# Performance work log

Hardware: AMD Instinct MI355X
Metric: run time of the kernel (lower is better)

The kernel has to match this reference:

```python
import jax, jax.numpy as jnp
import numpy as np

B, H, N, D = 16, 8, 256, 32


def setup_inputs() -> dict:
    key = jax.random.key(0)
    k1, k2, k3 = jax.random.split(key, 3)
    q = jax.random.normal(k1, (B, H, N, D), dtype=jnp.float32)
    k = jax.random.normal(k2, (B, H, N, D), dtype=jnp.float32)
    scale = jnp.ones((1,), dtype=jnp.float32)  # unused by the module
    mask = jnp.zeros((B, 1, N, N), dtype=bool)  # True == masked out
    # learned attention vector, xavier_uniform over (1, H, 1, 1, D)
    fan = 1 * H * 1 * 1 * D
    bound = float(np.sqrt(6.0 / (1 + D)))  # xavier for (..., D) param
    attention = jax.random.uniform(k3, (1, H, 1, 1, D), dtype=jnp.float32,
                                   minval=-bound, maxval=bound)
    return {"q": q, "k": k, "scale": scale, "mask": mask, "attention": attention}


def reference(q, k, scale, mask, attention):
    # summed: [B, H, Nq, Nk, D] via broadcast of q.unsqueeze(-2)+k.unsqueeze(-3)
    summed = q[:, :, :, None, :] + k[:, :, None, :, :]
    # GATv2 score: a^T * silu(q_i + k_j), reduced over head_dim
    scores = jnp.sum(jax.nn.silu(summed) * attention, axis=-1)  # [B, H, Nq, Nk]
    neg = jnp.finfo(scores.dtype).min
    scores_masked = jnp.where(mask, neg, scores)
    attn = jax.nn.softmax(scores_masked, axis=-1)
    return attn
```

## Files before the change

### kernel.cpp

```cpp
#include <hip/hip_runtime.h>
#include <stdint.h>
#include <stddef.h>

constexpr int Bc = 16, Hc = 8, Nc = 256, Dc = 32;
constexpr float LOG2E = 1.44269504088896340736f;

constexpr int    MF    = 10;
constexpr double PHALF = 9.7;
constexpr double LFIT  = 9.0;

constexpr double PI_ = 3.14159265358979323846;

constexpr double cexp_(double x) {
    int n = (int)(x >= 0 ? x + 0.5 : x - 0.5);
    double f = x - n, t = 1.0, s = 1.0;
    for (int i = 1; i <= 26; ++i) { t *= f / i; s += t; }
    const double E = 2.71828182845904523536;
    double en = 1.0, bb = n >= 0 ? E : 1.0 / E;
    int an = n < 0 ? -n : n;
    for (int i = 0; i < an; ++i) en *= bb;
    return s * en;
}
constexpr double creduce_(double x) {
    while (x >  PI_) x -= 2.0 * PI_;
    while (x < -PI_) x += 2.0 * PI_;
    return x;
}
constexpr double ccos_(double x0) {
    double x = creduce_(x0), x2 = x * x, t = 1.0, s = 1.0;
    for (int i = 1; i <= 16; ++i) { t *= -x2 / ((2.0*i - 1.0) * (2.0*i)); s += t; }
    return s;
}
constexpr double csin_(double x0) {
    double x = creduce_(x0), x2 = x * x, t = x, s = x;
    for (int i = 1; i <= 16; ++i) { t *= -x2 / ((2.0*i) * (2.0*i + 1.0)); s += t; }
    return s;
}
constexpr double Gfun_(double x) {
    double z = x < 0 ? -x : x;
    double e = cexp_(z);
    return 0.5 * z * ((e - 1.0) / (e + 1.0));
}
constexpr double csqrt_(double x) {
    if (x <= 0) return 0;
    double r = x > 1 ? x : 1;
    for (int i = 0; i < 40; ++i) r = 0.5 * (r + x / r);
    return r;
}

struct FitT { float tk[MF + 1]; float tq[MF + 1]; };

constexpr FitT lsFit_() {
    constexpr int NB = MF + 1;
    double A[NB][NB] = {}, bv[NB] = {};
    for (int p = 0; p < NB; ++p)
        for (int qq = 0; qq < NB; ++qq) {
            double wm = (p - qq) * PI_ / PHALF, wp = (p + qq) * PI_ / PHALF;
            double Sm = (p == qq)     ? LFIT : csin_(wm * LFIT) / wm;
            double Sp = (p + qq == 0) ? LFIT : csin_(wp * LFIT) / wp;
            A[p][qq] = 0.5 * (Sm + Sp);
        }
    constexpr int NS = 128;
    double hh = LFIT / NS, gx[NS + 1] = {};
    for (int i = 0; i <= NS; ++i) gx[i] = Gfun_(i * hh);
    for (int p = 0; p < NB; ++p) {
        double s = 0;
        for (int i = 0; i <= NS; ++i) {
            double wgt = (i == 0 || i == NS) ? 1.0 : ((i & 1) ? 4.0 : 2.0);
            s += wgt * gx[i] * ccos_(p * PI_ / PHALF * (i * hh));
        }
        bv[p] = s * hh / 3.0;
    }
    for (int p = 0; p < NB; ++p) A[p][p] += 1e-8 * LFIT;
    for (int col = 0; col < NB; ++col) {
        int piv = col; double best = A[col][col] < 0 ? -A[col][col] : A[col][col];
        for (int r = col + 1; r < NB; ++r) {
            double v = A[r][col] < 0 ? -A[r][col] : A[r][col];
            if (v > best) { best = v; piv = r; }
        }
        if (piv != col) {
            for (int cc = 0; cc < NB; ++cc) { double t = A[col][cc]; A[col][cc] = A[piv][cc]; A[piv][cc] = t; }
            double t = bv[col]; bv[col] = bv[piv]; bv[piv] = t;
        }
        for (int r = col + 1; r < NB; ++r) {
            double f = A[r][col] / A[col][col];
            for (int cc = col; cc < NB; ++cc) A[r][cc] -= f * A[col][cc];
            bv[r] -= f * bv[col];
        }
    }
    double c[NB] = {};
    for (int r = NB - 1; r >= 0; --r) {
        double s = bv[r];
        for (int cc = r + 1; cc < NB; ++cc) s -= A[r][cc] * c[cc];
        c[r] = s / A[r][r];
    }
    FitT f{};
    for (int m = 0; m <= MF; ++m) {
        double rt = csqrt_(c[m] < 0 ? -c[m] : c[m]);
        f.tk[m] = (float)rt;
        f.tq[m] = (float)(c[m] < 0 ? -rt : rt);
    }
    return f;
}
constexpr FitT CF = lsFit_();

typedef _Float16 half8  __attribute__((ext_vector_type(8)));
typedef float    f32x16 __attribute__((ext_vector_type(16)));

__device__ __forceinline__ uint32_t pkh_(float a, float b) {
    auto v = __builtin_amdgcn_cvt_pkrtz(a, b);
    uint32_t u; __builtin_memcpy(&u, &v, 4); return u;
}

__device__ __forceinline__ void dma16(const char* g, char* l) {
    __builtin_amdgcn_global_load_lds(
        (const __attribute__((address_space(1))) unsigned int*)(g),
        (__attribute__((address_space(3))) unsigned int*)(l),
        16, 0, 0);
}

constexpr int    KCH      = Nc * 128;
constexpr size_t KF_BYTES = (size_t)Bc * Hc * MF * KCH;
constexpr size_t AK_OFF   = KF_BYTES;

__global__ __launch_bounds__(256) void feat_kernel(
    const float* __restrict__ k, const float* __restrict__ att,
    char* __restrict__ kf, float* __restrict__ akg)
{
    const int gid = blockIdx.x * 256 + threadIdx.x;
    const int u  = gid & 7;
    const int j  = (gid >> 3) & (Nc - 1);
    const int bh = gid >> 11;
    const int h  = bh & (Hc - 1);
    const float4 kv = *(const float4*)(k + ((size_t)bh * Nc + j) * Dc + 4 * u);
    const float4 a4 = *(const float4*)(att + h * Dc + 4 * u);
    float part = a4.x * kv.x + a4.y * kv.y + a4.z * kv.z + a4.w * kv.w;
    part += __shfl_xor(part, 1, 64);
    part += __shfl_xor(part, 2, 64);
    part += __shfl_xor(part, 4, 64);
    if (u == 0) akg[bh * Nc + j] = part;

    const float invTwoP = (float)(1.0 / (2.0 * PHALF));
    float c1[4], s1[4], cm[4], sm[4];
    const float rv[4] = { kv.x, kv.y, kv.z, kv.w };
#pragma unroll
    for (int c = 0; c < 4; ++c) {
        float r = __builtin_amdgcn_fractf(rv[c] * invTwoP);
        c1[c] = __builtin_amdgcn_cosf(r);
        s1[c] = __builtin_amdgcn_sinf(r);
        cm[c] = c1[c]; sm[c] = s1[c];
    }
    char* base = kf + (size_t)bh * (MF * KCH) + j * 128 + ((u ^ (j & 7)) << 4);
#pragma unroll
    for (int m = 1; m <= MF; ++m) {
        const float tk = CF.tk[m];
        uint4 wv;
        wv.x = pkh_(tk * cm[0], tk * sm[0]);
        wv.y = pkh_(tk * cm[1], tk * sm[1]);
        wv.z = pkh_(tk * cm[2], tk * sm[2]);
        wv.w = pkh_(tk * cm[3], tk * sm[3]);
        *(uint4*)(base + (size_t)(m - 1) * KCH) = wv;
        if (m < MF) {
#pragma unroll
            for (int e = 0; e < 4; ++e) {
                float cn = fmaf(c1[e], cm[e], -(s1[e] * sm[e]));
                float sn = fmaf(s1[e], cm[e],   c1[e] * sm[e]);
                cm[e] = cn; sm[e] = sn;
            }
        }
    }
}

constexpr int QCH   = 128 * 128;
constexpr int QBASE = 2 * KCH;
constexpr int SRED  = QBASE + 2 * QCH;
constexpr int SMEM2 = SRED + 2048;

__global__ __launch_bounds__(512, 2) void gatv2_gemm_kernel(
    const float* __restrict__ q, const uint8_t* __restrict__ mask,
    const float* __restrict__ att, const char* __restrict__ kf,
    const float* __restrict__ akg, float* __restrict__ out)
{
    extern __shared__ char smem[];
    float* sred = (float*)(smem + SRED);
    const int tid = threadIdx.x, lane = tid & 63, w = tid >> 6;
    const int bh = blockIdx.y, h = bh & 7, b = bh >> 3;
    const int iBlk = blockIdx.x * 128;
    const float invTwoP = (float)(1.0 / (2.0 * PHALF));

    const int dq = tid & 7, rw = tid >> 3;
    const float4 a4 = *(const float4*)(att + h * Dc + 4 * dq);
    float qc1[8], qs1[8], qcm[8], qsm[8];
    int offQ[2];
#pragma unroll
    for (int it = 0; it < 2; ++it) {
        const int i = rw + it * 64;
        const float4 qv = *(const float4*)(q + ((size_t)bh * Nc + iBlk + i) * Dc + 4 * dq);
        const float rv[4] = { qv.x, qv.y, qv.z, qv.w };
#pragma unroll
        for (int c = 0; c < 4; ++c) {
            float r = __builtin_amdgcn_fractf(rv[c] * invTwoP);
            qc1[4*it+c] = __builtin_amdgcn_cosf(r);
            qs1[4*it+c] = __builtin_amdgcn_sinf(r);
            qcm[4*it+c] = qc1[4*it+c];
            qsm[4*it+c] = qs1[4*it+c];
        }
        offQ[it] = QBASE + i * 128 + ((dq ^ (i & 7)) << 4);
    }

    const char* kg = kf + (size_t)bh * (MF * KCH) + w * 4096 + lane * 16;

    auto dmaK = [&](int mIdx, int buf) {
        const char* g = kg + (size_t)mIdx * KCH;
        char* l = smem + buf * KCH + w * 4096;
#pragma unroll
        for (int t = 0; t < 4; ++t)
            dma16(g + t * 1024, l + t * 1024);
    };

    auto buildQ = [&](int m, int buf) {
        const float g0 = CF.tq[m]*a4.x, g1 = CF.tq[m]*a4.y;
        const float g2 = CF.tq[m]*a4.z, g3 = CF.tq[m]*a4.w;
#pragma unroll
        for (int it = 0; it < 2; ++it) {
            uint4 wv;
            wv.x = pkh_(g0*qcm[4*it+0], -(g0*qsm[4*it+0]));
            wv.y = pkh_(g1*qcm[4*it+1], -(g1*qsm[4*it+1]));
            wv.z = pkh_(g2*qcm[4*it+2], -(g2*qsm[4*it+2]));
            wv.w = pkh_(g3*qcm[4*it+3], -(g3*qsm[4*it+3]));
            *(uint4*)(smem + buf * QCH + offQ[it]) = wv;
        }
        if (m < MF) {
#pragma unroll
            for (int e = 0; e < 8; ++e) {
                float cn = fmaf(qc1[e], qcm[e], -(qs1[e] * qsm[e]));
                float sn = fmaf(qs1[e], qcm[e],   qc1[e] * qsm[e]);
                qcm[e] = cn; qsm[e] = sn;
            }
        }
    };

    const int hi5 = lane >> 5, col = lane & 31;
    const int wi = w & 1, wj = w >> 1;
    const int baseA0 = QBASE + (wi*64 + col) * 128, baseA1 = baseA0 + 32*128;
    const int baseB0 = (wj*64 + col) * 128,         baseB1 = baseB0 + 32*128;
    const int sA = col & 7;

    f32x16 acc[2][2];
#pragma unroll
    for (int a2 = 0; a2 < 2; ++a2)
#pragma unroll
        for (int b2 = 0; b2 < 2; ++b2)
#pragma unroll
            for (int e = 0; e < 16; ++e) acc[a2][b2][e] = 0.0f;

    auto mfmaC = [&](int buf) {
        const int qb = buf * QCH, kb = buf * KCH;
#pragma unroll
        for (int s = 0; s < 4; ++s) {
            const int du = ((2*s + hi5) ^ sA) << 4;
            half8 A0 = *(const half8*)(smem + qb + baseA0 + du);
            half8 A1 = *(const half8*)(smem + qb + baseA1 + du);
            half8 B0 = *(const half8*)(smem + kb + baseB0 + du);
            half8 B1 = *(const half8*)(smem + kb + baseB1 + du);
            acc[0][0] = __builtin_amdgcn_mfma_f32_32x32x16_f16(A0, B0, acc[0][0], 0, 0, 0);
            acc[0][1] = __builtin_amdgcn_mfma_f32_32x32x16_f16(A0, B1, acc[0][1], 0, 0, 0);
            acc[1][0] = __builtin_amdgcn_mfma_f32_32x32x16_f16(A1, B0, acc[1][0], 0, 0, 0);
            acc[1][1] = __builtin_amdgcn_mfma_f32_32x32x16_f16(A1, B1, acc[1][1], 0, 0, 0);
        }
    };

    buildQ(1, 0);
    dmaK(0, 0);
    __syncthreads();
#pragma unroll
    for (int m = 1; m <= MF; ++m) {
        const int cur = (m - 1) & 1;
        if (m < MF) { dmaK(m, 1 - cur); buildQ(m + 1, 1 - cur); }
        mfmaC(cur);
        __syncthreads();
    }

    constexpr float M0 = 24.0f;
    const int jB = wj * 64;
    const float akj0 = akg[bh * Nc + jB + col];
    const float akj1 = akg[bh * Nc + jB + 32 + col];
    const int iB = iBlk + wi * 64;

#pragma unroll
    for (int it2 = 0; it2 < 2; ++it2)
#pragma unroll
        for (int e = 0; e < 16; ++e) {
            int rloc = (e & 3) + 8 * (e >> 2) + 4 * hi5;
            int ig = iB + it2 * 32 + rloc;
            const uint8_t* mr = mask + ((size_t)(b * Nc + ig)) * Nc + jB + col;
            float v0 = fmaf(0.5f, akj0, acc[it2][0][e]);
            float v1 = fmaf(0.5f, akj1, acc[it2][1][e]);
            if (mr[0])  v0 = -1.0e30f;
            if (mr[32]) v1 = -1.0e30f;
            float p0 = __builtin_amdgcn_exp2f(__builtin_fminf((v0 - M0) * LOG2E, 80.0f));
            float p1 = __builtin_amdgcn_exp2f(__builtin_fminf((v1 - M0) * LOG2E, 80.0f));
            acc[it2][0][e] = p0;
            acc[it2][1][e] = p1;
            float sm = p0 + p1;
#pragma unroll
            for (int off = 1; off < 32; off <<= 1) sm += __shfl_xor(sm, off, 64);
            if (col == e) sred[(wi * 64 + it2 * 32 + rloc) * 4 + wj] = sm;
        }
    __syncthreads();

    float* obase = out + (size_t)bh * Nc * Nc;
#pragma unroll
    for (int it2 = 0; it2 < 2; ++it2)
#pragma unroll
        for (int e = 0; e < 16; ++e) {
            int rloc = (e & 3) + 8 * (e >> 2) + 4 * hi5;
            int iL = wi * 64 + it2 * 32 + rloc;
            int ig = iB + it2 * 32 + rloc;
            float4 tv = *(const float4*)(&sred[iL * 4]);
            float inv = __builtin_amdgcn_rcpf(tv.x + tv.y + tv.z + tv.w);
            obase[(size_t)ig * Nc + jB + col]      = acc[it2][0][e] * inv;
            obase[(size_t)ig * Nc + jB + 32 + col] = acc[it2][1][e] * inv;
        }
}

extern "C" void kernel_launch(void* const* d_in, const int* in_sizes, int n_in,
                              void* d_out, int out_size, void* d_ws, size_t ws_size,
                              hipStream_t stream) {
    const float*   q    = (const float*)d_in[0];
    const float*   k    = (const float*)d_in[1];
    const uint8_t* mask = (const uint8_t*)d_in[3];
    const float*   att  = (const float*)d_in[4];
    float*         out  = (float*)d_out;

    char*  kfbuf = (char*)d_ws;
    float* akg   = (float*)((char*)d_ws + AK_OFF);

    feat_kernel<<<dim3((Bc * Hc * Nc * 8) / 256), dim3(256), 0, stream>>>(
        k, att, kfbuf, akg);

    (void)hipFuncSetAttribute((const void*)gatv2_gemm_kernel,
                              hipFuncAttributeMaxDynamicSharedMemorySize, SMEM2);
    dim3 grid(2, Bc * Hc);
    gatv2_gemm_kernel<<<grid, dim3(512), SMEM2, stream>>>(
        q, mask, att, kfbuf, akg, out);
}
```

Measured before the change: 112.4 us.

## Precompute Q Fourier features in feat kernel and DMA them alongside K

Moves the per-harmonic Q feature construction (sin/cos recurrence, scaling by attention weights, fp16 packing) out of the GEMM kernel into the feature kernel, which now writes both K and Q feature planes to workspace. The GEMM kernel then streams both operands into LDS with direct global-to-LDS loads in one double-buffered pipeline. This removes VALU work and register pressure from the GEMM main loop. In exchange it adds a second workspace plane of Q features and extra global traffic to write and re-read it.

```diff
diff --git a/kernel.cpp b/kernel.cpp
--- a/kernel.cpp
+++ b/kernel.cpp
@@ -119,131 +119,116 @@
         16, 0, 0);
 }
 
-constexpr int    KCH      = Nc * 128;
-constexpr size_t KF_BYTES = (size_t)Bc * Hc * MF * KCH;
-constexpr size_t AK_OFF   = KF_BYTES;
+constexpr int    KCH    = Nc * 128;
+constexpr size_t QF_OFF = (size_t)Bc * Hc * MF * KCH;
+constexpr size_t AK_OFF = 2 * QF_OFF;
 
 __global__ __launch_bounds__(256) void feat_kernel(
-    const float* __restrict__ k, const float* __restrict__ att,
-    char* __restrict__ kf, float* __restrict__ akg)
+    const float* __restrict__ q, const float* __restrict__ k,
+    const float* __restrict__ att, char* __restrict__ ws, float* __restrict__ akg)
 {
     const int gid = blockIdx.x * 256 + threadIdx.x;
     const int u  = gid & 7;
-    const int j  = (gid >> 3) & (Nc - 1);
+    const int r  = (gid >> 3) & (Nc - 1);
     const int bh = gid >> 11;
     const int h  = bh & (Hc - 1);
-    const float4 kv = *(const float4*)(k + ((size_t)bh * Nc + j) * Dc + 4 * u);
     const float4 a4 = *(const float4*)(att + h * Dc + 4 * u);
+    const float invTwoP = (float)(1.0 / (2.0 * PHALF));
+
+    const float4 kv = *(const float4*)(k + ((size_t)bh * Nc + r) * Dc + 4 * u);
     float part = a4.x * kv.x + a4.y * kv.y + a4.z * kv.z + a4.w * kv.w;
     part += __shfl_xor(part, 1, 64);
     part += __shfl_xor(part, 2, 64);
     part += __shfl_xor(part, 4, 64);
-    if (u == 0) akg[bh * Nc + j] = part;
-
-    const float invTwoP = (float)(1.0 / (2.0 * PHALF));
-    float c1[4], s1[4], cm[4], sm[4];
-    const float rv[4] = { kv.x, kv.y, kv.z, kv.w };
+    if (u == 0) akg[bh * Nc + r] = part;
+
+    float kc1[4], ks1[4], kcm[4], ksm[4];
+    const float krv[4] = { kv.x, kv.y, kv.z, kv.w };
 #pragma unroll
     for (int c = 0; c < 4; ++c) {
-        float r = __builtin_amdgcn_fractf(rv[c] * invTwoP);
-        c1[c] = __builtin_amdgcn_cosf(r);
-        s1[c] = __builtin_amdgcn_sinf(r);
-        cm[c] = c1[c]; sm[c] = s1[c];
-    }
-    char* base = kf + (size_t)bh * (MF * KCH) + j * 128 + ((u ^ (j & 7)) << 4);
+        float rr = __builtin_amdgcn_fractf(krv[c] * invTwoP);
+        kc1[c] = __builtin_amdgcn_cosf(rr);
+        ks1[c] = __builtin_amdgcn_sinf(rr);
+        kcm[c] = kc1[c]; ksm[c] = ks1[c];
+    }
+    const float4 qv = *(const float4*)(q + ((size_t)bh * Nc + r) * Dc + 4 * u);
+    float qc1[4], qs1[4], qcm[4], qsm[4];
+    const float qrv[4] = { qv.x, qv.y, qv.z, qv.w };
+#pragma unroll
+    for (int c = 0; c < 4; ++c) {
+        float rr = __builtin_amdgcn_fractf(qrv[c] * invTwoP);
+        qc1[c] = __builtin_amdgcn_cosf(rr);
+        qs1[c] = __builtin_amdgcn_sinf(rr);
+        qcm[c] = qc1[c]; qsm[c] = qs1[c];
+    }
+
+    char* kb = ws + (size_t)bh * (MF * KCH) + r * 128 + ((u ^ (r & 7)) << 4);
+    char* qb = kb + QF_OFF;
 #pragma unroll
     for (int m = 1; m <= MF; ++m) {
         const float tk = CF.tk[m];
-        uint4 wv;
-        wv.x = pkh_(tk * cm[0], tk * sm[0]);
-        wv.y = pkh_(tk * cm[1], tk * sm[1]);
-        wv.z = pkh_(tk * cm[2], tk * sm[2]);
-        wv.w = pkh_(tk * cm[3], tk * sm[3]);
-        *(uint4*)(base + (size_t)(m - 1) * KCH) = wv;
+        const float g0 = CF.tq[m] * a4.x, g1 = CF.tq[m] * a4.y;
+        const float g2 = CF.tq[m] * a4.z, g3 = CF.tq[m] * a4.w;
+        uint4 wk, wq;
+        wk.x = pkh_(tk * kcm[0], tk * ksm[0]);
+        wk.y = pkh_(tk * kcm[1], tk * ksm[1]);
+        wk.z = pkh_(tk * kcm[2], tk * ksm[2]);
+        wk.w = pkh_(tk * kcm[3], tk * ksm[3]);
+        wq.x = pkh_(g0 * qcm[0], -(g0 * qsm[0]));
+        wq.y = pkh_(g1 * qcm[1], -(g1 * qsm[1]));
+        wq.z = pkh_(g2 * qcm[2], -(g2 * qsm[2]));
+        wq.w = pkh_(g3 * qcm[3], -(g3 * qsm[3]));
+        *(uint4*)(kb + (size_t)(m - 1) * KCH) = wk;
+        *(uint4*)(qb + (size_t)(m - 1) * KCH) = wq;
         if (m < MF) {
 #pragma unroll
             for (int e = 0; e < 4; ++e) {
-                float cn = fmaf(c1[e], cm[e], -(s1[e] * sm[e]));
-                float sn = fmaf(s1[e], cm[e],   c1[e] * sm[e]);
-                cm[e] = cn; sm[e] = sn;
+                float cn = fmaf(kc1[e], kcm[e], -(ks1[e] * ksm[e]));
+                float sn = fmaf(ks1[e], kcm[e],   kc1[e] * ksm[e]);
+                kcm[e] = cn; ksm[e] = sn;
+                cn = fmaf(qc1[e], qcm[e], -(qs1[e] * qsm[e]));
+                sn = fmaf(qs1[e], qcm[e],   qc1[e] * qsm[e]);
+                qcm[e] = cn; qsm[e] = sn;
             }
         }
     }
 }
 
-constexpr int QCH   = 128 * 128;
-constexpr int QBASE = 2 * KCH;
-constexpr int SRED  = QBASE + 2 * QCH;
+constexpr int BUF   = 48 * 1024;
+constexpr int SRED  = 2 * BUF;
 constexpr int SMEM2 = SRED + 2048;
 
 __global__ __launch_bounds__(512, 2) void gatv2_gemm_kernel(
-    const float* __restrict__ q, const uint8_t* __restrict__ mask,
-    const float* __restrict__ att, const char* __restrict__ kf,
+    const uint8_t* __restrict__ mask, const char* __restrict__ ws,
     const float* __restrict__ akg, float* __restrict__ out)
 {
     extern __shared__ char smem[];
     float* sred = (float*)(smem + SRED);
     const int tid = threadIdx.x, lane = tid & 63, w = tid >> 6;
-    const int bh = blockIdx.y, h = bh & 7, b = bh >> 3;
+    const int bh = blockIdx.y, b = bh >> 3;
     const int iBlk = blockIdx.x * 128;
-    const float invTwoP = (float)(1.0 / (2.0 * PHALF));
-
-    const int dq = tid & 7, rw = tid >> 3;
-    const float4 a4 = *(const float4*)(att + h * Dc + 4 * dq);
-    float qc1[8], qs1[8], qcm[8], qsm[8];
-    int offQ[2];
-#pragma unroll
-    for (int it = 0; it < 2; ++it) {
-        const int i = rw + it * 64;
-        const float4 qv = *(const float4*)(q + ((size_t)bh * Nc + iBlk + i) * Dc + 4 * dq);
-        const float rv[4] = { qv.x, qv.y, qv.z, qv.w };
-#pragma unroll
-        for (int c = 0; c < 4; ++c) {
-            float r = __builtin_amdgcn_fractf(rv[c] * invTwoP);
-            qc1[4*it+c] = __builtin_amdgcn_cosf(r);
-            qs1[4*it+c] = __builtin_amdgcn_sinf(r);
-            qcm[4*it+c] = qc1[4*it+c];
-            qsm[4*it+c] = qs1[4*it+c];
-        }
-        offQ[it] = QBASE + i * 128 + ((dq ^ (i & 7)) << 4);
-    }
-
-    const char* kg = kf + (size_t)bh * (MF * KCH) + w * 4096 + lane * 16;
-
-    auto dmaK = [&](int mIdx, int buf) {
-        const char* g = kg + (size_t)mIdx * KCH;
-        char* l = smem + buf * KCH + w * 4096;
+
+    const char* kfB = ws + (size_t)bh * (MF * KCH) + w * 4096 + lane * 16;
+    const char* qfB = ws + QF_OFF + (size_t)bh * (MF * KCH) + iBlk * 128
+                      + w * 2048 + lane * 16;
+
+    auto dmaC = [&](int m, int buf) {
+        const char* gk = kfB + (size_t)m * KCH;
+        char* lk = smem + buf * BUF + w * 4096;
 #pragma unroll
         for (int t = 0; t < 4; ++t)
-            dma16(g + t * 1024, l + t * 1024);
-    };
-
-    auto buildQ = [&](int m, int buf) {
-        const float g0 = CF.tq[m]*a4.x, g1 = CF.tq[m]*a4.y;
-        const float g2 = CF.tq[m]*a4.z, g3 = CF.tq[m]*a4.w;
-#pragma unroll
-        for (int it = 0; it < 2; ++it) {
-            uint4 wv;
-            wv.x = pkh_(g0*qcm[4*it+0], -(g0*qsm[4*it+0]));
-            wv.y = pkh_(g1*qcm[4*it+1], -(g1*qsm[4*it+1]));
-            wv.z = pkh_(g2*qcm[4*it+2], -(g2*qsm[4*it+2]));
-            wv.w = pkh_(g3*qcm[4*it+3], -(g3*qsm[4*it+3]));
-            *(uint4*)(smem + buf * QCH + offQ[it]) = wv;
-        }
-        if (m < MF) {
-#pragma unroll
-            for (int e = 0; e < 8; ++e) {
-                float cn = fmaf(qc1[e], qcm[e], -(qs1[e] * qsm[e]));
-                float sn = fmaf(qs1[e], qcm[e],   qc1[e] * qsm[e]);
-                qcm[e] = cn; qsm[e] = sn;
-            }
-        }
+            dma16(gk + t * 1024, lk + t * 1024);
+        const char* gq = qfB + (size_t)m * KCH;
+        char* lq = smem + buf * BUF + 32768 + w * 2048;
+#pragma unroll
+        for (int t = 0; t < 2; ++t)
+            dma16(gq + t * 1024, lq + t * 1024);
     };
 
     const int hi5 = lane >> 5, col = lane & 31;
     const int wi = w & 1, wj = w >> 1;
-    const int baseA0 = QBASE + (wi*64 + col) * 128, baseA1 = baseA0 + 32*128;
-    const int baseB0 = (wj*64 + col) * 128,         baseB1 = baseB0 + 32*128;
+    const int baseA0 = 32768 + (wi * 64 + col) * 128, baseA1 = baseA0 + 32 * 128;
+    const int baseB0 = (wj * 64 + col) * 128,         baseB1 = baseB0 + 32 * 128;
     const int sA = col & 7;
 
     f32x16 acc[2][2];
@@ -255,14 +240,14 @@
             for (int e = 0; e < 16; ++e) acc[a2][b2][e] = 0.0f;
 
     auto mfmaC = [&](int buf) {
-        const int qb = buf * QCH, kb = buf * KCH;
+        const int o = buf * BUF;
 #pragma unroll
         for (int s = 0; s < 4; ++s) {
-            const int du = ((2*s + hi5) ^ sA) << 4;
-            half8 A0 = *(const half8*)(smem + qb + baseA0 + du);
-            half8 A1 = *(const half8*)(smem + qb + baseA1 + du);
-            half8 B0 = *(const half8*)(smem + kb + baseB0 + du);
-            half8 B1 = *(const half8*)(smem + kb + baseB1 + du);
+            const int du = ((2 * s + hi5) ^ sA) << 4;
+            half8 A0 = *(const half8*)(smem + o + baseA0 + du);
+            half8 A1 = *(const half8*)(smem + o + baseA1 + du);
+            half8 B0 = *(const half8*)(smem + o + baseB0 + du);
+            half8 B1 = *(const half8*)(smem + o + baseB1 + du);
             acc[0][0] = __builtin_amdgcn_mfma_f32_32x32x16_f16(A0, B0, acc[0][0], 0, 0, 0);
             acc[0][1] = __builtin_amdgcn_mfma_f32_32x32x16_f16(A0, B1, acc[0][1], 0, 0, 0);
             acc[1][0] = __builtin_amdgcn_mfma_f32_32x32x16_f16(A1, B0, acc[1][0], 0, 0, 0);
@@ -270,13 +255,12 @@
         }
     };
 
-    buildQ(1, 0);
-    dmaK(0, 0);
+    dmaC(0, 0);
     __syncthreads();
 #pragma unroll
-    for (int m = 1; m <= MF; ++m) {
-        const int cur = (m - 1) & 1;
-        if (m < MF) { dmaK(m, 1 - cur); buildQ(m + 1, 1 - cur); }
+    for (int m = 0; m < MF; ++m) {
+        const int cur = m & 1;
+        if (m + 1 < MF) dmaC(m + 1, 1 - cur);
         mfmaC(cur);
         __syncthreads();
     }
@@ -333,15 +317,14 @@
     const float*   att  = (const float*)d_in[4];
     float*         out  = (float*)d_out;
 
-    char*  kfbuf = (char*)d_ws;
-    float* akg   = (float*)((char*)d_ws + AK_OFF);
+    char*  wsb = (char*)d_ws;
+    float* akg = (float*)(wsb + AK_OFF);
 
     feat_kernel<<<dim3((Bc * Hc * Nc * 8) / 256), dim3(256), 0, stream>>>(
-        k, att, kfbuf, akg);
+        q, k, att, wsb, akg);
 
     (void)hipFuncSetAttribute((const void*)gatv2_gemm_kernel,
                               hipFuncAttributeMaxDynamicSharedMemorySize, SMEM2);
     dim3 grid(2, Bc * Hc);
-    gatv2_gemm_kernel<<<grid, dim3(512), SMEM2, stream>>>(
-        q, mask, att, kfbuf, akg, out);
-}
+    gatv2_gemm_kernel<<<grid, dim3(512), SMEM2, stream>>>(mask, wsb, akg, out);
+}
```

Result: slower. 119.6 us (+6.4%).
